# Performance work log

Hardware: AMD Instinct MI355X
Metric: run time of the kernel (lower is better)

## Reference

```python
import jax, jax.numpy as jnp
import numpy as np

N_NODES = 50000
N_EDGES = 800000
D_IN = 128
D_OUT = 128


def setup_inputs() -> dict:
    key = jax.random.key(0)
    k1, k2, k3, k4, k5 = jax.random.split(key, 5)
    gain = float(np.sqrt(2.0))  # calculate_gain('relu')
    # xavier_uniform bound: gain * sqrt(6/(fan_in+fan_out))
    bound = gain * float(np.sqrt(6.0 / (D_IN + D_OUT)))
    feat = jax.random.normal(k1, (N_NODES, D_IN), dtype=jnp.float32)
    weight = jax.random.uniform(k2, (D_IN, D_OUT), minval=-bound, maxval=bound, dtype=jnp.float32)
    loop_weight = jax.random.uniform(k3, (D_IN, D_OUT), minval=-bound, maxval=bound, dtype=jnp.float32)
    h_bias = jnp.zeros((D_OUT,), dtype=jnp.float32)
    src = jax.random.randint(k4, (N_EDGES,), 0, N_NODES, dtype=jnp.int32)
    dst = jax.random.randint(k5, (N_EDGES,), 0, N_NODES, dtype=jnp.int32)
    return {"feat": feat, "weight": weight, "h_bias": h_bias,
            "loop_weight": loop_weight, "src": src, "dst": dst}


def reference(feat, weight, h_bias, loop_weight, src, dst):
    # message: m_e = feat[src_e] @ W ; aggregate: h_v = sum_{e: dst_e=v} m_e
    # (equivalently transform-then-gather, which avoids the [E, D] matmul)
    transformed = feat @ weight                    # [N, D_out]
    msgs = transformed[src]                        # [E, D_out] gather
    h = jax.ops.segment_sum(msgs, dst, num_segments=feat.shape[0])  # [N, D_out]
    h = h + h_bias                                 # bias
    h = h + feat @ loop_weight                     # self-loop
    # activation=None, dropout=0 -> identity
    return h
```

## Files before the change

kernel.cpp:

```cpp
#include <hip/hip_runtime.h>

#define D 128
#define CAP 64
#define FCHUNK 2048
#define LROW 264

typedef __attribute__((ext_vector_type(8))) short bf16x8;
typedef __attribute__((ext_vector_type(4))) float f32x4;

__device__ inline unsigned short f2bf_rne(float x) {
    unsigned u = __float_as_uint(x);
    return (unsigned short)((u + 0x7FFFu + ((u >> 16) & 1u)) >> 16);
}
__device__ inline float bf_lo(unsigned u) { return __uint_as_float(u << 16); }
__device__ inline float bf_hi(unsigned u) { return __uint_as_float(u & 0xFFFF0000u); }

__global__ __launch_bounds__(256) void prep_kernel(
    const float* __restrict__ W, const float* __restrict__ LW,
    unsigned short* __restrict__ Bt, int* __restrict__ cursor, int ncur)
{
    int tid = blockIdx.x * 256 + threadIdx.x;
    if (tid < 2 * D * D) {
        int n = tid >> 7;
        int k = tid & 127;
        float v = (n < D) ? W[(size_t)k * D + n] : LW[(size_t)k * D + (n - D)];
        Bt[(size_t)n * D + k] = f2bf_rne(v);
    }
    int j = tid - 2 * D * D;
    if (j >= 0 && j < ncur) cursor[j] = 0;
}

__global__ __launch_bounds__(256) void fill_kernel(
    const int* __restrict__ src, const int* __restrict__ dst,
    int* __restrict__ cursor, unsigned short* __restrict__ ebuf,
    int E, int cstride)
{
    const int chunk = blockIdx.x >> 3;
    const int cls   = blockIdx.x & 7;
    const int base  = chunk * FCHUNK + threadIdx.x;

#pragma unroll
    for (int ii = 0; ii < FCHUNK / 256; ++ii) {
        const int e  = base + ii * 256;
        const bool ok = (e < E);
        const int d = ok ? dst[e] : -1;
        const int s = ok ? src[e] : 0;
        if (ok && (d & 7) == cls) {
            const int pos = atomicAdd(&cursor[(cls * cstride) + (d >> 3)], 1);
            if (pos < CAP) ebuf[(size_t)d * CAP + pos] = (unsigned short)s;
        }
    }
}

__global__ __launch_bounds__(256) void mfma_transform(
    const float* __restrict__ feat, const unsigned short* __restrict__ Bt,
    unsigned short* __restrict__ T2, int N)
{
    __shared__ unsigned short tile[4 * 16 * LROW];
    const int wave = threadIdx.x >> 6;
    const int lane = threadIdx.x & 63;
    const int wrow0 = blockIdx.x * 64 + wave * 16;
    const int m    = lane & 15;
    const int kg   = lane >> 4;

    int arow_idx = wrow0 + m;
    if (arow_idx >= N) arow_idx = N - 1;
    const float* arow = feat + (size_t)arow_idx * D;

    bf16x8 a[4];
#pragma unroll
    for (int ks = 0; ks < 4; ++ks) {
        const float4 f0 = *(const float4*)(arow + ks * 32 + kg * 8);
        const float4 f1 = *(const float4*)(arow + ks * 32 + kg * 8 + 4);
        bf16x8 v;
        v[0] = (short)f2bf_rne(f0.x); v[1] = (short)f2bf_rne(f0.y);
        v[2] = (short)f2bf_rne(f0.z); v[3] = (short)f2bf_rne(f0.w);
        v[4] = (short)f2bf_rne(f1.x); v[5] = (short)f2bf_rne(f1.y);
        v[6] = (short)f2bf_rne(f1.z); v[7] = (short)f2bf_rne(f1.w);
        a[ks] = v;
    }

    f32x4 acc[16];
#pragma unroll
    for (int t = 0; t < 16; ++t) acc[t] = (f32x4){0.f, 0.f, 0.f, 0.f};

#pragma unroll
    for (int t = 0; t < 16; ++t) {
        const unsigned short* brow = Bt + (size_t)(t * 16 + m) * D;
        bf16x8 b0 = *(const bf16x8*)(brow + 0 * 32 + kg * 8);
        bf16x8 b1 = *(const bf16x8*)(brow + 1 * 32 + kg * 8);
        bf16x8 b2 = *(const bf16x8*)(brow + 2 * 32 + kg * 8);
        bf16x8 b3 = *(const bf16x8*)(brow + 3 * 32 + kg * 8);
        acc[t] = __builtin_amdgcn_mfma_f32_16x16x32_bf16(a[0], b0, acc[t], 0, 0, 0);
        acc[t] = __builtin_amdgcn_mfma_f32_16x16x32_bf16(a[1], b1, acc[t], 0, 0, 0);
        acc[t] = __builtin_amdgcn_mfma_f32_16x16x32_bf16(a[2], b2, acc[t], 0, 0, 0);
        acc[t] = __builtin_amdgcn_mfma_f32_16x16x32_bf16(a[3], b3, acc[t], 0, 0, 0);
    }

    unsigned short* wtile = tile + wave * 16 * LROW;
#pragma unroll
    for (int t = 0; t < 16; ++t) {
#pragma unroll
        for (int r = 0; r < 4; ++r)
            wtile[(kg * 4 + r) * LROW + t * 16 + m] = f2bf_rne(acc[t][r]);
    }

#pragma unroll
    for (int i = 0; i < 8; ++i) {
        const int f   = i * 64 + lane;
        const int row = f >> 5;
        const int cs  = f & 31;
        if (wrow0 + row < N) {
            const uint4 v = *(const uint4*)(wtile + row * LROW + cs * 8);
            *(uint4*)(T2 + (size_t)(wrow0 + row) * 256 + cs * 8) = v;
        }
    }
}

__global__ __launch_bounds__(256) void gather_kernel(
    const unsigned short* __restrict__ ebuf, const int* __restrict__ cursor,
    const unsigned short* __restrict__ T2, const float* __restrict__ bias,
    float* __restrict__ out, int N, int cstride)
{
    const int cls  = blockIdx.x & 7;
    const int w    = threadIdx.x >> 6;
    const int node = (((int)(blockIdx.x >> 3) * 4 + w) * 8) + cls;
    const int lane = threadIdx.x & 63;
    if (node >= N) return;

    const int h = lane >> 5;
    const int q = lane & 31;

    int deg = cursor[(cls * cstride) + (node >> 3)];
    if (deg > CAP) deg = CAP;

    const unsigned* region = (const unsigned*)(ebuf + (size_t)node * CAP);
    const unsigned short* Tq = T2 + q * 4;

    float a0 = 0.f, a1 = 0.f, a2 = 0.f, a3 = 0.f;

    for (int j = 0; j < deg; j += 16) {
        uint2 u[8];
#pragma unroll
        for (int k = 0; k < 8; ++k) {
            const unsigned w32 = region[(j >> 1) + k];
            unsigned s = h ? (w32 >> 16) : (w32 & 0xFFFFu);
            if (j + 2 * k + h >= deg) s = 0;
            u[k] = *(const uint2*)(Tq + (size_t)s * 256);
        }
#pragma unroll
        for (int k = 0; k < 8; ++k) {
            const bool live = (j + 2 * k + h) < deg;
            a0 += live ? bf_lo(u[k].x) : 0.f;
            a1 += live ? bf_hi(u[k].x) : 0.f;
            a2 += live ? bf_lo(u[k].y) : 0.f;
            a3 += live ? bf_hi(u[k].y) : 0.f;
        }
    }

    a0 += __shfl_xor(a0, 32, 64);
    a1 += __shfl_xor(a1, 32, 64);
    a2 += __shfl_xor(a2, 32, 64);
    a3 += __shfl_xor(a3, 32, 64);

    if (h == 0) {
        const uint2 sv = *(const uint2*)(T2 + (size_t)node * 256 + 128 + q * 4);
        const float4 b = *(const float4*)(bias + q * 4);
        f32x4 o;
        o.x = b.x + bf_lo(sv.x) + a0;
        o.y = b.y + bf_hi(sv.x) + a1;
        o.z = b.z + bf_lo(sv.y) + a2;
        o.w = b.w + bf_hi(sv.y) + a3;
        __builtin_nontemporal_store(o, (f32x4*)(out + (size_t)node * D + q * 4));
    }
}

extern "C" void kernel_launch(void* const* d_in, const int* in_sizes, int n_in,
                              void* d_out, int out_size, void* d_ws, size_t ws_size,
                              hipStream_t stream) {
    const float* feat = (const float*)d_in[0];
    const float* W    = (const float*)d_in[1];
    const float* bias = (const float*)d_in[2];
    const float* LW   = (const float*)d_in[3];
    const int*   src  = (const int*)d_in[4];
    const int*   dst  = (const int*)d_in[5];
    float* out = (float*)d_out;

    const int N = in_sizes[0] / D;
    const int E = in_sizes[4];
    const int cstride = (N + 7) >> 3;
    const int ncur = 8 * cstride;

    unsigned short* T2   = (unsigned short*)d_ws;
    unsigned short* Bt   = T2 + (size_t)N * 256;
    unsigned short* ebuf = Bt + 2 * D * D;
    int* cursor = (int*)(ebuf + (size_t)N * CAP);

    {
        const int work = 2 * D * D + ncur;
        prep_kernel<<<dim3((work + 255) / 256), 256, 0, stream>>>(W, LW, Bt, cursor, ncur);
    }

    {
        const int nchunks = (E + FCHUNK - 1) / FCHUNK;
        fill_kernel<<<dim3(nchunks * 8), 256, 0, stream>>>(src, dst, cursor, ebuf, E, cstride);
    }

    mfma_transform<<<dim3((N + 63) / 64), 256, 0, stream>>>(feat, Bt, T2, N);

    {
        const int bpc = (cstride + 3) / 4;
        gather_kernel<<<dim3(8 * bpc), 256, 0, stream>>>(
            ebuf, cursor, T2, bias, out, N, cstride);
    }
}
```

Baseline: 187.6 us.

## Merge four kernels into one persistent cooperative kernel with grid syncs

Replaces the prep, fill, transform and gather launches with a single cooperative persistent kernel that loops over work units and separates phases with grid-wide syncs. The transform and fill phases now run back-to-back without a barrier between them. The transform is split into four 64-column passes with a smaller shared tile so register and LDS pressure permit six blocks per CU. This aims to remove launch gaps and inter-kernel drain, at the cost of grid-sync overhead and a fixed grid size that may limit latency hiding in the gather phase.

```diff
diff --git a/kernel.cpp b/kernel.cpp
--- a/kernel.cpp
+++ b/kernel.cpp
@@ -1,9 +1,10 @@
 #include <hip/hip_runtime.h>
+#include <hip/hip_cooperative_groups.h>
 
 #define D 128
 #define CAP 64
-#define FCHUNK 2048
-#define LROW 264
+#define FCHUNK 512
+#define TPAD 68
 
 typedef __attribute__((ext_vector_type(8))) short bf16x8;
 typedef __attribute__((ext_vector_type(4))) float f32x4;
@@ -15,163 +16,174 @@
 __device__ inline float bf_lo(unsigned u) { return __uint_as_float(u << 16); }
 __device__ inline float bf_hi(unsigned u) { return __uint_as_float(u & 0xFFFF0000u); }
 
-__global__ __launch_bounds__(256) void prep_kernel(
-    const float* __restrict__ W, const float* __restrict__ LW,
-    unsigned short* __restrict__ Bt, int* __restrict__ cursor, int ncur)
+__global__ __launch_bounds__(256, 6) void mega_kernel(
+    const float* __restrict__ feat, const float* __restrict__ W,
+    const float* __restrict__ bias, const float* __restrict__ LW,
+    const int* __restrict__ src, const int* __restrict__ dst,
+    float* __restrict__ out,
+    unsigned short* __restrict__ T2, unsigned short* __restrict__ Bt,
+    unsigned short* __restrict__ ebuf, int* __restrict__ cursor,
+    int N, int E, int cstride)
 {
-    int tid = blockIdx.x * 256 + threadIdx.x;
-    if (tid < 2 * D * D) {
-        int n = tid >> 7;
-        int k = tid & 127;
-        float v = (n < D) ? W[(size_t)k * D + n] : LW[(size_t)k * D + (n - D)];
-        Bt[(size_t)n * D + k] = f2bf_rne(v);
-    }
-    int j = tid - 2 * D * D;
-    if (j >= 0 && j < ncur) cursor[j] = 0;
-}
-
-__global__ __launch_bounds__(256) void fill_kernel(
-    const int* __restrict__ src, const int* __restrict__ dst,
-    int* __restrict__ cursor, unsigned short* __restrict__ ebuf,
-    int E, int cstride)
-{
-    const int chunk = blockIdx.x >> 3;
-    const int cls   = blockIdx.x & 7;
-    const int base  = chunk * FCHUNK + threadIdx.x;
-
-#pragma unroll
-    for (int ii = 0; ii < FCHUNK / 256; ++ii) {
-        const int e  = base + ii * 256;
-        const bool ok = (e < E);
-        const int d = ok ? dst[e] : -1;
-        const int s = ok ? src[e] : 0;
-        if (ok && (d & 7) == cls) {
-            const int pos = atomicAdd(&cursor[(cls * cstride) + (d >> 3)], 1);
-            if (pos < CAP) ebuf[(size_t)d * CAP + pos] = (unsigned short)s;
-        }
-    }
-}
-
-__global__ __launch_bounds__(256) void mfma_transform(
-    const float* __restrict__ feat, const unsigned short* __restrict__ Bt,
-    unsigned short* __restrict__ T2, int N)
-{
-    __shared__ unsigned short tile[4 * 16 * LROW];
-    const int wave = threadIdx.x >> 6;
-    const int lane = threadIdx.x & 63;
-    const int wrow0 = blockIdx.x * 64 + wave * 16;
-    const int m    = lane & 15;
-    const int kg   = lane >> 4;
-
-    int arow_idx = wrow0 + m;
-    if (arow_idx >= N) arow_idx = N - 1;
-    const float* arow = feat + (size_t)arow_idx * D;
-
-    bf16x8 a[4];
-#pragma unroll
-    for (int ks = 0; ks < 4; ++ks) {
-        const float4 f0 = *(const float4*)(arow + ks * 32 + kg * 8);
-        const float4 f1 = *(const float4*)(arow + ks * 32 + kg * 8 + 4);
-        bf16x8 v;
-        v[0] = (short)f2bf_rne(f0.x); v[1] = (short)f2bf_rne(f0.y);
-        v[2] = (short)f2bf_rne(f0.z); v[3] = (short)f2bf_rne(f0.w);
-        v[4] = (short)f2bf_rne(f1.x); v[5] = (short)f2bf_rne(f1.y);
-        v[6] = (short)f2bf_rne(f1.z); v[7] = (short)f2bf_rne(f1.w);
-        a[ks] = v;
-    }
-
-    f32x4 acc[16];
-#pragma unroll
-    for (int t = 0; t < 16; ++t) acc[t] = (f32x4){0.f, 0.f, 0.f, 0.f};
-
-#pragma unroll
-    for (int t = 0; t < 16; ++t) {
-        const unsigned short* brow = Bt + (size_t)(t * 16 + m) * D;
-        bf16x8 b0 = *(const bf16x8*)(brow + 0 * 32 + kg * 8);
-        bf16x8 b1 = *(const bf16x8*)(brow + 1 * 32 + kg * 8);
-        bf16x8 b2 = *(const bf16x8*)(brow + 2 * 32 + kg * 8);
-        bf16x8 b3 = *(const bf16x8*)(brow + 3 * 32 + kg * 8);
-        acc[t] = __builtin_amdgcn_mfma_f32_16x16x32_bf16(a[0], b0, acc[t], 0, 0, 0);
-        acc[t] = __builtin_amdgcn_mfma_f32_16x16x32_bf16(a[1], b1, acc[t], 0, 0, 0);
-        acc[t] = __builtin_amdgcn_mfma_f32_16x16x32_bf16(a[2], b2, acc[t], 0, 0, 0);
-        acc[t] = __builtin_amdgcn_mfma_f32_16x16x32_bf16(a[3], b3, acc[t], 0, 0, 0);
-    }
-
-    unsigned short* wtile = tile + wave * 16 * LROW;
-#pragma unroll
-    for (int t = 0; t < 16; ++t) {
-#pragma unroll
-        for (int r = 0; r < 4; ++r)
-            wtile[(kg * 4 + r) * LROW + t * 16 + m] = f2bf_rne(acc[t][r]);
-    }
-
-#pragma unroll
-    for (int i = 0; i < 8; ++i) {
-        const int f   = i * 64 + lane;
-        const int row = f >> 5;
-        const int cs  = f & 31;
-        if (wrow0 + row < N) {
-            const uint4 v = *(const uint4*)(wtile + row * LROW + cs * 8);
-            *(uint4*)(T2 + (size_t)(wrow0 + row) * 256 + cs * 8) = v;
-        }
-    }
-}
-
-__global__ __launch_bounds__(256) void gather_kernel(
-    const unsigned short* __restrict__ ebuf, const int* __restrict__ cursor,
-    const unsigned short* __restrict__ T2, const float* __restrict__ bias,
-    float* __restrict__ out, int N, int cstride)
-{
-    const int cls  = blockIdx.x & 7;
-    const int w    = threadIdx.x >> 6;
-    const int node = (((int)(blockIdx.x >> 3) * 4 + w) * 8) + cls;
-    const int lane = threadIdx.x & 63;
-    if (node >= N) return;
-
-    const int h = lane >> 5;
-    const int q = lane & 31;
-
-    int deg = cursor[(cls * cstride) + (node >> 3)];
-    if (deg > CAP) deg = CAP;
-
-    const unsigned* region = (const unsigned*)(ebuf + (size_t)node * CAP);
-    const unsigned short* Tq = T2 + q * 4;
-
-    float a0 = 0.f, a1 = 0.f, a2 = 0.f, a3 = 0.f;
-
-    for (int j = 0; j < deg; j += 16) {
-        uint2 u[8];
-#pragma unroll
-        for (int k = 0; k < 8; ++k) {
-            const unsigned w32 = region[(j >> 1) + k];
-            unsigned s = h ? (w32 >> 16) : (w32 & 0xFFFFu);
-            if (j + 2 * k + h >= deg) s = 0;
-            u[k] = *(const uint2*)(Tq + (size_t)s * 256);
-        }
-#pragma unroll
-        for (int k = 0; k < 8; ++k) {
-            const bool live = (j + 2 * k + h) < deg;
-            a0 += live ? bf_lo(u[k].x) : 0.f;
-            a1 += live ? bf_hi(u[k].x) : 0.f;
-            a2 += live ? bf_lo(u[k].y) : 0.f;
-            a3 += live ? bf_hi(u[k].y) : 0.f;
-        }
-    }
-
-    a0 += __shfl_xor(a0, 32, 64);
-    a1 += __shfl_xor(a1, 32, 64);
-    a2 += __shfl_xor(a2, 32, 64);
-    a3 += __shfl_xor(a3, 32, 64);
-
-    if (h == 0) {
-        const uint2 sv = *(const uint2*)(T2 + (size_t)node * 256 + 128 + q * 4);
-        const float4 b = *(const float4*)(bias + q * 4);
-        f32x4 o;
-        o.x = b.x + bf_lo(sv.x) + a0;
-        o.y = b.y + bf_hi(sv.x) + a1;
-        o.z = b.z + bf_lo(sv.y) + a2;
-        o.w = b.w + bf_hi(sv.y) + a3;
-        __builtin_nontemporal_store(o, (f32x4*)(out + (size_t)node * D + q * 4));
+    __shared__ unsigned short tile[4 * 16 * TPAD];
+    const int tid  = threadIdx.x;
+    const int wave = tid >> 6;
+    const int lane = tid & 63;
+    const int G    = gridDim.x;
+
+    {
+        const int ncur = 8 * cstride;
+        const int work = 2 * D * D + ncur;
+        for (int i = blockIdx.x * 256 + tid; i < work; i += G * 256) {
+            if (i < 2 * D * D) {
+                const int n = i >> 7;
+                const int k = i & 127;
+                const float v = (n < D) ? W[(size_t)k * D + n] : LW[(size_t)k * D + (n - D)];
+                Bt[(size_t)n * D + k] = f2bf_rne(v);
+            } else {
+                cursor[i - 2 * D * D] = 0;
+            }
+        }
+    }
+    cooperative_groups::this_grid().sync();
+
+    {
+        const int ntiles = (N + 63) >> 6;
+        const int m  = lane & 15;
+        const int kg = lane >> 4;
+        unsigned short* wtile = tile + wave * 16 * TPAD;
+
+        for (int t64 = blockIdx.x; t64 < ntiles; t64 += G) {
+            const int wrow0 = t64 * 64 + wave * 16;
+            int arow_idx = wrow0 + m;
+            if (arow_idx >= N) arow_idx = N - 1;
+            const float* arow = feat + (size_t)arow_idx * D;
+
+            bf16x8 a[4];
+#pragma unroll
+            for (int ks = 0; ks < 4; ++ks) {
+                const float4 f0 = *(const float4*)(arow + ks * 32 + kg * 8);
+                const float4 f1 = *(const float4*)(arow + ks * 32 + kg * 8 + 4);
+                bf16x8 v;
+                v[0] = (short)f2bf_rne(f0.x); v[1] = (short)f2bf_rne(f0.y);
+                v[2] = (short)f2bf_rne(f0.z); v[3] = (short)f2bf_rne(f0.w);
+                v[4] = (short)f2bf_rne(f1.x); v[5] = (short)f2bf_rne(f1.y);
+                v[6] = (short)f2bf_rne(f1.z); v[7] = (short)f2bf_rne(f1.w);
+                a[ks] = v;
+            }
+
+#pragma unroll
+            for (int p = 0; p < 4; ++p) {
+                f32x4 acc[4];
+#pragma unroll
+                for (int tt = 0; tt < 4; ++tt) acc[tt] = (f32x4){0.f, 0.f, 0.f, 0.f};
+
+#pragma unroll
+                for (int tt = 0; tt < 4; ++tt) {
+                    const unsigned short* brow = Bt + (size_t)((p * 4 + tt) * 16 + m) * D;
+                    bf16x8 b0 = *(const bf16x8*)(brow + 0 * 32 + kg * 8);
+                    bf16x8 b1 = *(const bf16x8*)(brow + 1 * 32 + kg * 8);
+                    bf16x8 b2 = *(const bf16x8*)(brow + 2 * 32 + kg * 8);
+                    bf16x8 b3 = *(const bf16x8*)(brow + 3 * 32 + kg * 8);
+                    acc[tt] = __builtin_amdgcn_mfma_f32_16x16x32_bf16(a[0], b0, acc[tt], 0, 0, 0);
+                    acc[tt] = __builtin_amdgcn_mfma_f32_16x16x32_bf16(a[1], b1, acc[tt], 0, 0, 0);
+                    acc[tt] = __builtin_amdgcn_mfma_f32_16x16x32_bf16(a[2], b2, acc[tt], 0, 0, 0);
+                    acc[tt] = __builtin_amdgcn_mfma_f32_16x16x32_bf16(a[3], b3, acc[tt], 0, 0, 0);
+                }
+
+#pragma unroll
+                for (int tt = 0; tt < 4; ++tt)
+#pragma unroll
+                    for (int r = 0; r < 4; ++r)
+                        wtile[(kg * 4 + r) * TPAD + tt * 16 + m] = f2bf_rne(acc[tt][r]);
+
+#pragma unroll
+                for (int i = 0; i < 4; ++i) {
+                    const int f   = i * 64 + lane;
+                    const int row = f >> 4;
+                    const int seg = f & 15;
+                    if (wrow0 + row < N)
+                        *(uint2*)(T2 + (size_t)(wrow0 + row) * 256 + p * 64 + seg * 4) =
+                            *(const uint2*)(wtile + row * TPAD + seg * 4);
+                }
+            }
+        }
+    }
+
+    {
+        const int nunits = ((E + FCHUNK - 1) / FCHUNK) * 8;
+        for (int u = blockIdx.x; u < nunits; u += G) {
+            const int cls  = u & 7;
+            const int base = (u >> 3) * FCHUNK + tid;
+#pragma unroll
+            for (int ii = 0; ii < FCHUNK / 256; ++ii) {
+                const int e  = base + ii * 256;
+                const bool ok = (e < E);
+                const int d = ok ? dst[e] : -1;
+                const int s = ok ? src[e] : 0;
+                if (ok && (d & 7) == cls) {
+                    const int pos = atomicAdd(&cursor[cls * cstride + (d >> 3)], 1);
+                    if (pos < CAP) ebuf[(size_t)d * CAP + pos] = (unsigned short)s;
+                }
+            }
+        }
+    }
+    __threadfence();
+    cooperative_groups::this_grid().sync();
+
+    {
+        const int h = lane >> 5;
+        const int q = lane & 31;
+        const int nbiter = ((cstride + 3) >> 2) * 8;
+
+        for (int u = blockIdx.x; u < nbiter; u += G) {
+            const int cls  = u & 7;
+            const int node = (((u >> 3) * 4 + wave) * 8) + cls;
+            if (node >= N) continue;
+
+            int deg = cursor[cls * cstride + (node >> 3)];
+            if (deg > CAP) deg = CAP;
+
+            const unsigned* region = (const unsigned*)(ebuf + (size_t)node * CAP);
+            const unsigned short* Tq = T2 + q * 4;
+
+            float a0 = 0.f, a1 = 0.f, a2 = 0.f, a3 = 0.f;
+
+            for (int j = 0; j < deg; j += 16) {
+                uint2 uu[8];
+#pragma unroll
+                for (int k = 0; k < 8; ++k) {
+                    const unsigned w32 = region[(j >> 1) + k];
+                    unsigned s = h ? (w32 >> 16) : (w32 & 0xFFFFu);
+                    if (j + 2 * k + h >= deg) s = 0;
+                    uu[k] = *(const uint2*)(Tq + (size_t)s * 256);
+                }
+#pragma unroll
+                for (int k = 0; k < 8; ++k) {
+                    const bool live = (j + 2 * k + h) < deg;
+                    a0 += live ? bf_lo(uu[k].x) : 0.f;
+                    a1 += live ? bf_hi(uu[k].x) : 0.f;
+                    a2 += live ? bf_lo(uu[k].y) : 0.f;
+                    a3 += live ? bf_hi(uu[k].y) : 0.f;
+                }
+            }
+
+            a0 += __shfl_xor(a0, 32, 64);
+            a1 += __shfl_xor(a1, 32, 64);
+            a2 += __shfl_xor(a2, 32, 64);
+            a3 += __shfl_xor(a3, 32, 64);
+
+            if (h == 0) {
+                const uint2 sv = *(const uint2*)(T2 + (size_t)node * 256 + 128 + q * 4);
+                const float4 b = *(const float4*)(bias + q * 4);
+                f32x4 o;
+                o.x = b.x + bf_lo(sv.x) + a0;
+                o.y = b.y + bf_hi(sv.x) + a1;
+                o.z = b.z + bf_lo(sv.y) + a2;
+                o.w = b.w + bf_hi(sv.y) + a3;
+                __builtin_nontemporal_store(o, (f32x4*)(out + (size_t)node * D + q * 4));
+            }
+        }
     }
 }
 
@@ -186,31 +198,32 @@
     const int*   dst  = (const int*)d_in[5];
     float* out = (float*)d_out;
 
-    const int N = in_sizes[0] / D;
-    const int E = in_sizes[4];
-    const int cstride = (N + 7) >> 3;
-    const int ncur = 8 * cstride;
+    int N = in_sizes[0] / D;
+    int E = in_sizes[4];
+    int cstride = (N + 7) >> 3;
 
     unsigned short* T2   = (unsigned short*)d_ws;
     unsigned short* Bt   = T2 + (size_t)N * 256;
     unsigned short* ebuf = Bt + 2 * D * D;
     int* cursor = (int*)(ebuf + (size_t)N * CAP);
 
-    {
-        const int work = 2 * D * D + ncur;
-        prep_kernel<<<dim3((work + 255) / 256), 256, 0, stream>>>(W, LW, Bt, cursor, ncur);
-    }
-
-    {
-        const int nchunks = (E + FCHUNK - 1) / FCHUNK;
-        fill_kernel<<<dim3(nchunks * 8), 256, 0, stream>>>(src, dst, cursor, ebuf, E, cstride);
-    }
-
-    mfma_transform<<<dim3((N + 63) / 64), 256, 0, stream>>>(feat, Bt, T2, N);
-
-    {
-        const int bpc = (cstride + 3) / 4;
-        gather_kernel<<<dim3(8 * bpc), 256, 0, stream>>>(
-            ebuf, cursor, T2, bias, out, N, cstride);
-    }
+    static int G = 0;
+    if (G == 0) {
+        int nb = 0;
+        hipOccupancyMaxActiveBlocksPerMultiprocessor(&nb, (const void*)mega_kernel, 256, 0);
+        int dev = 0;
+        hipGetDevice(&dev);
+        hipDeviceProp_t prop;
+        hipGetDeviceProperties(&prop, dev);
+        int g = nb * prop.multiProcessorCount;
+        if (g < 8) g = 8;
+        G = g & ~7;
+    }
+
+    void* args[] = { (void*)&feat, (void*)&W, (void*)&bias, (void*)&LW,
+                     (void*)&src, (void*)&dst, (void*)&out,
+                     (void*)&T2, (void*)&Bt, (void*)&ebuf, (void*)&cursor,
+                     (void*)&N, (void*)&E, (void*)&cstride };
+    hipLaunchCooperativeKernel((const void*)mega_kernel, dim3(G), dim3(256),
+                               args, 0, stream);
 }
```

New measurement: 519.6 us. 177% more time.

## Fuse edge-bucketing fill and MFMA transform into one concurrent launch

Applied to the files above, without the earlier changes.

Merges the edge fill kernel and the MFMA feature transform into a single grid. The first block range does the transform and the remaining blocks do the atomic edge bucketing, so the two independent stages can overlap and one launch disappears. The transform now works in four passes of four output tiles, with a smaller LDS staging tile and launch bounds requesting 8 blocks per CU, to cut register and LDS use and raise occupancy. The trade-off is more, narrower global stores and mixed block types competing for the same CUs.

```diff
diff --git a/kernel.cpp b/kernel.cpp
--- a/kernel.cpp
+++ b/kernel.cpp
@@ -3,7 +3,7 @@
 #define D 128
 #define CAP 64
 #define FCHUNK 2048
-#define LROW 264
+#define TPAD 68
 
 typedef __attribute__((ext_vector_type(8))) short bf16x8;
 typedef __attribute__((ext_vector_type(4))) float f32x4;
@@ -30,38 +30,40 @@
     if (j >= 0 && j < ncur) cursor[j] = 0;
 }
 
-__global__ __launch_bounds__(256) void fill_kernel(
+__global__ __launch_bounds__(256, 8) void fill_mfma_kernel(
     const int* __restrict__ src, const int* __restrict__ dst,
     int* __restrict__ cursor, unsigned short* __restrict__ ebuf,
-    int E, int cstride)
-{
-    const int chunk = blockIdx.x >> 3;
-    const int cls   = blockIdx.x & 7;
-    const int base  = chunk * FCHUNK + threadIdx.x;
-
-#pragma unroll
-    for (int ii = 0; ii < FCHUNK / 256; ++ii) {
-        const int e  = base + ii * 256;
-        const bool ok = (e < E);
-        const int d = ok ? dst[e] : -1;
-        const int s = ok ? src[e] : 0;
-        if (ok && (d & 7) == cls) {
-            const int pos = atomicAdd(&cursor[(cls * cstride) + (d >> 3)], 1);
-            if (pos < CAP) ebuf[(size_t)d * CAP + pos] = (unsigned short)s;
-        }
-    }
-}
-
-__global__ __launch_bounds__(256) void mfma_transform(
+    int E, int cstride, int nmfma,
     const float* __restrict__ feat, const unsigned short* __restrict__ Bt,
     unsigned short* __restrict__ T2, int N)
 {
-    __shared__ unsigned short tile[4 * 16 * LROW];
+    __shared__ unsigned short tile[4 * 16 * TPAD];
+    const int b = blockIdx.x;
+
+    if (b >= nmfma) {
+        const int fidx = b - nmfma;
+        const int cls  = b & 7;
+        const int base = (fidx >> 3) * FCHUNK + threadIdx.x;
+#pragma unroll
+        for (int ii = 0; ii < FCHUNK / 256; ++ii) {
+            const int e  = base + ii * 256;
+            const bool ok = (e < E);
+            const int d = ok ? dst[e] : -1;
+            const int s = ok ? src[e] : 0;
+            if (ok && (d & 7) == cls) {
+                const int pos = atomicAdd(&cursor[cls * cstride + (d >> 3)], 1);
+                if (pos < CAP) ebuf[(size_t)d * CAP + pos] = (unsigned short)s;
+            }
+        }
+        return;
+    }
+
     const int wave = threadIdx.x >> 6;
     const int lane = threadIdx.x & 63;
-    const int wrow0 = blockIdx.x * 64 + wave * 16;
-    const int m    = lane & 15;
-    const int kg   = lane >> 4;
+    const int wrow0 = b * 64 + wave * 16;
+    const int m  = lane & 15;
+    const int kg = lane >> 4;
+    unsigned short* wtile = tile + wave * 16 * TPAD;
 
     int arow_idx = wrow0 + m;
     if (arow_idx >= N) arow_idx = N - 1;
@@ -80,39 +82,39 @@
         a[ks] = v;
     }
 
-    f32x4 acc[16];
-#pragma unroll
-    for (int t = 0; t < 16; ++t) acc[t] = (f32x4){0.f, 0.f, 0.f, 0.f};
-
-#pragma unroll
-    for (int t = 0; t < 16; ++t) {
-        const unsigned short* brow = Bt + (size_t)(t * 16 + m) * D;
-        bf16x8 b0 = *(const bf16x8*)(brow + 0 * 32 + kg * 8);
-        bf16x8 b1 = *(const bf16x8*)(brow + 1 * 32 + kg * 8);
-        bf16x8 b2 = *(const bf16x8*)(brow + 2 * 32 + kg * 8);
-        bf16x8 b3 = *(const bf16x8*)(brow + 3 * 32 + kg * 8);
-        acc[t] = __builtin_amdgcn_mfma_f32_16x16x32_bf16(a[0], b0, acc[t], 0, 0, 0);
-        acc[t] = __builtin_amdgcn_mfma_f32_16x16x32_bf16(a[1], b1, acc[t], 0, 0, 0);
-        acc[t] = __builtin_amdgcn_mfma_f32_16x16x32_bf16(a[2], b2, acc[t], 0, 0, 0);
-        acc[t] = __builtin_amdgcn_mfma_f32_16x16x32_bf16(a[3], b3, acc[t], 0, 0, 0);
-    }
-
-    unsigned short* wtile = tile + wave * 16 * LROW;
-#pragma unroll
-    for (int t = 0; t < 16; ++t) {
-#pragma unroll
-        for (int r = 0; r < 4; ++r)
-            wtile[(kg * 4 + r) * LROW + t * 16 + m] = f2bf_rne(acc[t][r]);
-    }
-
-#pragma unroll
-    for (int i = 0; i < 8; ++i) {
-        const int f   = i * 64 + lane;
-        const int row = f >> 5;
-        const int cs  = f & 31;
-        if (wrow0 + row < N) {
-            const uint4 v = *(const uint4*)(wtile + row * LROW + cs * 8);
-            *(uint4*)(T2 + (size_t)(wrow0 + row) * 256 + cs * 8) = v;
+#pragma unroll
+    for (int p = 0; p < 4; ++p) {
+        f32x4 acc[4];
+#pragma unroll
+        for (int tt = 0; tt < 4; ++tt) acc[tt] = (f32x4){0.f, 0.f, 0.f, 0.f};
+
+#pragma unroll
+        for (int tt = 0; tt < 4; ++tt) {
+            const unsigned short* brow = Bt + (size_t)((p * 4 + tt) * 16 + m) * D;
+            bf16x8 b0 = *(const bf16x8*)(brow + 0 * 32 + kg * 8);
+            bf16x8 b1 = *(const bf16x8*)(brow + 1 * 32 + kg * 8);
+            bf16x8 b2 = *(const bf16x8*)(brow + 2 * 32 + kg * 8);
+            bf16x8 b3 = *(const bf16x8*)(brow + 3 * 32 + kg * 8);
+            acc[tt] = __builtin_amdgcn_mfma_f32_16x16x32_bf16(a[0], b0, acc[tt], 0, 0, 0);
+            acc[tt] = __builtin_amdgcn_mfma_f32_16x16x32_bf16(a[1], b1, acc[tt], 0, 0, 0);
+            acc[tt] = __builtin_amdgcn_mfma_f32_16x16x32_bf16(a[2], b2, acc[tt], 0, 0, 0);
+            acc[tt] = __builtin_amdgcn_mfma_f32_16x16x32_bf16(a[3], b3, acc[tt], 0, 0, 0);
+        }
+
+#pragma unroll
+        for (int tt = 0; tt < 4; ++tt)
+#pragma unroll
+            for (int r = 0; r < 4; ++r)
+                wtile[(kg * 4 + r) * TPAD + tt * 16 + m] = f2bf_rne(acc[tt][r]);
+
+#pragma unroll
+        for (int i = 0; i < 4; ++i) {
+            const int f   = i * 64 + lane;
+            const int row = f >> 4;
+            const int seg = f & 15;
+            if (wrow0 + row < N)
+                *(uint2*)(T2 + (size_t)(wrow0 + row) * 256 + p * 64 + seg * 4) =
+                    *(const uint2*)(wtile + row * TPAD + seg * 4);
         }
     }
 }
@@ -131,7 +133,7 @@
     const int h = lane >> 5;
     const int q = lane & 31;
 
-    int deg = cursor[(cls * cstride) + (node >> 3)];
+    int deg = cursor[cls * cstride + (node >> 3)];
     if (deg > CAP) deg = CAP;
 
     const unsigned* region = (const unsigned*)(ebuf + (size_t)node * CAP);
@@ -203,10 +205,11 @@
 
     {
         const int nchunks = (E + FCHUNK - 1) / FCHUNK;
-        fill_kernel<<<dim3(nchunks * 8), 256, 0, stream>>>(src, dst, cursor, ebuf, E, cstride);
-    }
-
-    mfma_transform<<<dim3((N + 63) / 64), 256, 0, stream>>>(feat, Bt, T2, N);
+        const int nfill   = nchunks * 8;
+        const int nmfma   = (N + 63) / 64;
+        fill_mfma_kernel<<<dim3(nmfma + nfill), 256, 0, stream>>>(
+            src, dst, cursor, ebuf, E, cstride, nmfma, feat, Bt, T2, N);
+    }
 
     {
         const int bpc = (cstride + 3) / 4;
```

New measurement: 166.0 us. 1.13x faster.
